# Performance work log

Hardware: AMD Instinct MI355X
Metric: run time of the kernel (lower is better)

The kernel has to match this reference:

```python
import jax, jax.numpy as jnp
import numpy as np

N_HEADS = 12  # from init_kwargs


def setup_inputs() -> dict:
    key = jax.random.key(0)
    ks = jax.random.split(key, 9)
    d_model = 768
    c, s = 50, 4          # n_classes, n_synonyms
    b, t = 4, 1024        # batch, document length
    scale = 0.02
    return {
        "Q": jax.random.normal(ks[0], (c, s, d_model), jnp.float32),
        "H": jax.random.normal(ks[1], (b, t, d_model), jnp.float32),
        "ql": jax.random.normal(ks[2], (c, d_model), jnp.float32),
        "WQ_w": jax.random.normal(ks[3], (d_model, d_model), jnp.float32) * scale,
        "WQ_b": jax.random.normal(ks[4], (d_model,), jnp.float32) * scale,
        "WK_w": jax.random.normal(ks[5], (d_model, d_model), jnp.float32) * scale,
        "WK_b": jax.random.normal(ks[6], (d_model,), jnp.float32) * scale,
        "WV_w": jax.random.normal(ks[7], (d_model, d_model), jnp.float32) * scale,
        "WV_b": jax.random.normal(ks[8], (d_model,), jnp.float32) * scale,
    }


def reference(Q, H, ql, WQ_w, WQ_b, WK_w, WK_b, WV_w, WV_b):
    c, s, d_model = Q.shape
    b, t, _ = H.shape
    z, h = N_HEADS, d_model // N_HEADS  # heads, d_k

    # projections + split heads
    q_s = (Q @ WQ_w + WQ_b).reshape(c, s, z, h).transpose(0, 2, 1, 3)   # [c,z,s,h]
    k_s = jnp.tanh((H @ WK_w + WK_b).reshape(b, t, z, h).transpose(0, 2, 1, 3))  # [b,z,t,h]
    Kh = jnp.tanh(H.reshape(b, t, z, h).transpose(0, 2, 1, 3))          # [b,z,t,h]

    # custom 5D attention
    scores = jnp.einsum('bzth,czsh->bczst', k_s, q_s)                   # [b,c,z,s,t]
    attn = jax.nn.softmax(scores, axis=-1)
    context = jnp.einsum('bzth,bczst->bczsh', Kh, attn)                 # [b,c,z,s,h]
    context = context.mean(axis=3)                                      # AvgPool3d over s -> [b,c,z,h]

    Wql = ql @ WV_w + WV_b                                               # [c,d_model]
    output = jnp.einsum('bch,ch->bc', context.reshape(b, c, z * h), Wql)
    return output
```

## Files before the change

### kernel.cpp

```cpp
#include <hip/hip_runtime.h>
#include <hip/hip_bf16.h>
#include <cmath>


typedef __attribute__((ext_vector_type(8))) short bf8_t;
typedef __attribute__((ext_vector_type(4))) float f32x4;

__device__ inline unsigned short f2bf(float x) {
    unsigned u = __float_as_uint(x);
    return (unsigned short)((u + 0x7fffu + ((u >> 16) & 1u)) >> 16);
}
__device__ inline float ftanh(float x) {
    float t = __expf(2.f * x);
    return 1.f - 2.f * __builtin_amdgcn_rcpf(t + 1.f);
}

__global__ __launch_bounds__(256) void prep_kernel(
    const float* __restrict__ H, const float* __restrict__ WK,
    const float* __restrict__ WQ, const float* __restrict__ WV,
    const float* __restrict__ Q, const float* __restrict__ ql,
    unsigned short* __restrict__ Hbf,
    unsigned short* __restrict__ WTk, unsigned short* __restrict__ WTq,
    unsigned short* __restrict__ WTv,
    unsigned short* __restrict__ Qbf, unsigned short* __restrict__ qlbf)
{
    __shared__ unsigned short tile[64][72];
    const int bid = blockIdx.x, tid = threadIdx.x;
    if (bid < 1536) {
        int i = (bid * 256 + tid) * 8;
        float4 v0 = *(const float4*)&H[i];
        float4 v1 = *(const float4*)&H[i + 4];
        unsigned short h8[8] = {f2bf(v0.x), f2bf(v0.y), f2bf(v0.z), f2bf(v0.w),
                                f2bf(v1.x), f2bf(v1.y), f2bf(v1.z), f2bf(v1.w)};
        *(bf8_t*)&Hbf[i] = *(const bf8_t*)h8;
    } else if (bid < 1968) {
        int j = bid - 1536;
        int wsel = j / 144, l = j % 144;
        const float* W = (wsel == 0) ? WK : (wsel == 1) ? WQ : WV;
        unsigned short* WT = (wsel == 0) ? WTk : (wsel == 1) ? WTq : WTv;
        const int bn = (l % 12) * 64, bk = (l / 12) * 64;
        const int k = tid >> 4, n4 = (tid & 15) << 2;
#pragma unroll
        for (int i = 0; i < 4; i++) {
            int kk = k + i * 16;
            float4 v = *(const float4*)&W[(size_t)(bk + kk) * 768 + bn + n4];
            tile[n4 + 0][kk] = f2bf(v.x);
            tile[n4 + 1][kk] = f2bf(v.y);
            tile[n4 + 2][kk] = f2bf(v.z);
            tile[n4 + 3][kk] = f2bf(v.w);
        }
        __syncthreads();
#pragma unroll
        for (int i = 0; i < 2; i++) {
            int idx = tid + i * 256;
            int n = idx >> 3, k8 = (idx & 7) << 3;
            *(bf8_t*)&WT[(size_t)(bn + n) * 768 + bk + k8] = *(const bf8_t*)&tile[n][k8];
        }
    } else if (bid < 2043) {
        int i = ((bid - 1968) * 256 + tid) * 8;
        float4 v0 = *(const float4*)&Q[i];
        float4 v1 = *(const float4*)&Q[i + 4];
        unsigned short h8[8] = {f2bf(v0.x), f2bf(v0.y), f2bf(v0.z), f2bf(v0.w),
                                f2bf(v1.x), f2bf(v1.y), f2bf(v1.z), f2bf(v1.w)};
        *(bf8_t*)&Qbf[i] = *(const bf8_t*)h8;
    } else {
        int i = ((bid - 2043) * 256 + tid) * 8;
        if (i < 38400) {
            float4 v0 = *(const float4*)&ql[i];
            float4 v1 = *(const float4*)&ql[i + 4];
            unsigned short h8[8] = {f2bf(v0.x), f2bf(v0.y), f2bf(v0.z), f2bf(v0.w),
                                    f2bf(v1.x), f2bf(v1.y), f2bf(v1.z), f2bf(v1.w)};
            *(bf8_t*)&qlbf[i] = *(const bf8_t*)h8;
        }
    }
}

__global__ __launch_bounds__(256) void gemm_all_kernel(
    const unsigned short* __restrict__ Hbf, const unsigned short* __restrict__ Qbf,
    const unsigned short* __restrict__ qlbf,
    const unsigned short* __restrict__ WTk, const unsigned short* __restrict__ WTq,
    const unsigned short* __restrict__ WTv,
    const float* __restrict__ bk, const float* __restrict__ bq,
    const float* __restrict__ bv,
    unsigned short* __restrict__ KSb, unsigned short* __restrict__ QSbf,
    unsigned short* __restrict__ WQLbf)
{
    __shared__ unsigned short Al[128][72];
    __shared__ unsigned short Bl[64][72];
    int bid = blockIdx.x;
    const int tid = threadIdx.x;
    if (bid < 384) bid = (bid & 7) * 48 + (bid >> 3);
    int job, bm, bn, Mr, z = 0;
    const unsigned short *A, *B;
    const float* bias;
    if (bid < 384) {
        job = 0; z = bid % 12; bm = (bid / 12) * 128; bn = z * 64;
        A = Hbf; B = WTk; bias = bk; Mr = 4096;
    } else if (bid < 408) {
        int l = bid - 384;
        job = 1; bm = (l / 12) * 128; bn = (l % 12) * 64;
        A = Qbf; B = WTq; bias = bq; Mr = 200;
    } else {
        job = 2; bm = 0; bn = (bid - 408) * 64;
        A = qlbf; B = WTv; bias = bv; Mr = 50;
    }
    const int lane = tid & 63, w = tid >> 6;
    const int wm = (w & 1) * 64, wn = (w >> 1) * 32;
    const int fr = lane & 15, fg = lane >> 4;

    f32x4 acc[4][2] = {};

    for (int k0 = 0; k0 < 768; k0 += 64) {
#pragma unroll
        for (int i = 0; i < 4; i++) {
            int f = tid + i * 256;
            int r = f >> 3, c8 = (f & 7) << 3;
            bf8_t v = {};
            if (bm + r < Mr)
                v = *(const bf8_t*)&A[(size_t)(bm + r) * 768 + k0 + c8];
            *(bf8_t*)&Al[r][c8] = v;
        }
#pragma unroll
        for (int i = 0; i < 2; i++) {
            int f = tid + i * 256;
            int r = f >> 3, c8 = (f & 7) << 3;
            *(bf8_t*)&Bl[r][c8] = *(const bf8_t*)&B[(size_t)(bn + r) * 768 + k0 + c8];
        }
        __syncthreads();
#pragma unroll
        for (int kk = 0; kk < 2; kk++) {
            bf8_t a[4], bb[2];
#pragma unroll
            for (int mt = 0; mt < 4; mt++)
                a[mt] = *(const bf8_t*)&Al[wm + mt * 16 + fr][kk * 32 + fg * 8];
#pragma unroll
            for (int nt = 0; nt < 2; nt++)
                bb[nt] = *(const bf8_t*)&Bl[wn + nt * 16 + fr][kk * 32 + fg * 8];
#pragma unroll
            for (int mt = 0; mt < 4; mt++)
#pragma unroll
                for (int nt = 0; nt < 2; nt++)
                    acc[mt][nt] = __builtin_amdgcn_mfma_f32_16x16x32_bf16(
                        a[mt], bb[nt], acc[mt][nt], 0, 0, 0);
        }
        __syncthreads();
    }
#pragma unroll
    for (int nt = 0; nt < 2; nt++) {
        int ng = bn + wn + nt * 16 + fr;
        float bvv = bias[ng];
        if (job == 0) {
            int hh = ng & 63;
#pragma unroll
            for (int mt = 0; mt < 4; mt++) {
#pragma unroll
                for (int r = 0; r < 4; r++) {
                    int rg = bm + wm + mt * 16 + fg * 4 + r;
                    int bb2 = rg >> 10, t = rg & 1023;
                    KSb[(((size_t)bb2 * 12 + z) * 1024 + t) * 64 + hh] =
                        f2bf(ftanh(acc[mt][nt][r] + bvv));
                }
            }
        } else {
            unsigned short* outp = (job == 1) ? QSbf : WQLbf;
            int Mw = (job == 1) ? 208 : 64;
#pragma unroll
            for (int mt = 0; mt < 4; mt++) {
#pragma unroll
                for (int r = 0; r < 4; r++) {
                    int rg = bm + wm + mt * 16 + fg * 4 + r;
                    if (rg < Mw)
                        outp[(size_t)rg * 768 + ng] = f2bf(acc[mt][nt][r] + bvv);
                }
            }
        }
    }
}

__global__ __launch_bounds__(256) void attn7_kernel(
    const unsigned short* __restrict__ KSb, const unsigned short* __restrict__ QSbf,
    const float* __restrict__ H, const unsigned short* __restrict__ WQLbf,
    float* __restrict__ pd, float* __restrict__ pn)
{
    __shared__ unsigned short KTl[128][72];
    __shared__ unsigned short Wl[64][72];
    __shared__ float kwl[128][50];
    const int blk = blockIdx.x;
    const int ts = blk & 7;
    const int z  = (blk >> 3) % 12;
    const int b  = blk / 96;
    const int tid = threadIdx.x;
    const int lane = tid & 63, w = tid >> 6;
    const int fr = lane & 15, fg = lane >> 4;

    const float* hb = H + ((size_t)(b * 1024 + ts * 128)) * 768 + z * 64;
#pragma unroll
    for (int i = 0; i < 4; i++) {
        int f = tid + i * 256;
        int r = f >> 3, c8 = (f & 7) << 3;
        float4 v0 = *(const float4*)&hb[(size_t)r * 768 + c8];
        float4 v1 = *(const float4*)&hb[(size_t)r * 768 + c8 + 4];
        unsigned short t8[8] = {f2bf(ftanh(v0.x)), f2bf(ftanh(v0.y)),
                                f2bf(ftanh(v0.z)), f2bf(ftanh(v0.w)),
                                f2bf(ftanh(v1.x)), f2bf(ftanh(v1.y)),
                                f2bf(ftanh(v1.z)), f2bf(ftanh(v1.w))};
        *(bf8_t*)&KTl[r][c8] = *(const bf8_t*)t8;
    }
#pragma unroll
    for (int i = 0; i < 2; i++) {
        int f = tid + i * 256;
        int r = f >> 3, c8 = (f & 7) << 3;
        *(bf8_t*)&Wl[r][c8] = *(const bf8_t*)&WQLbf[(size_t)r * 768 + z * 64 + c8];
    }
    __syncthreads();

    {
        const int wm = w * 32;
        f32x4 acc[2][4] = {};
#pragma unroll
        for (int kk = 0; kk < 2; kk++) {
            bf8_t a[2], bb[4];
#pragma unroll
            for (int mt = 0; mt < 2; mt++)
                a[mt] = *(const bf8_t*)&KTl[wm + mt * 16 + fr][kk * 32 + fg * 8];
#pragma unroll
            for (int nt = 0; nt < 4; nt++)
                bb[nt] = *(const bf8_t*)&Wl[nt * 16 + fr][kk * 32 + fg * 8];
#pragma unroll
            for (int mt = 0; mt < 2; mt++)
#pragma unroll
                for (int nt = 0; nt < 4; nt++)
                    acc[mt][nt] = __builtin_amdgcn_mfma_f32_16x16x32_bf16(
                        a[mt], bb[nt], acc[mt][nt], 0, 0, 0);
        }
#pragma unroll
        for (int nt = 0; nt < 4; nt++) {
            int c = nt * 16 + fr;
            if (c < 50) {
#pragma unroll
                for (int mt = 0; mt < 2; mt++)
#pragma unroll
                    for (int r = 0; r < 4; r++)
                        kwl[wm + mt * 16 + fg * 4 + r][c] = acc[mt][nt][r];
            }
        }
    }
    __syncthreads();

    const unsigned short* ksb = KSb + ((size_t)((b * 12 + z) * 1024) + ts * 128) * 64;
#pragma unroll
    for (int i = 0; i < 4; i++) {
        int f = tid + i * 256;
        int r = f >> 3, c8 = (f & 7) << 3;
        *(bf8_t*)&KTl[r][c8] = *(const bf8_t*)&ksb[(size_t)r * 64 + c8];
    }
    __syncthreads();

    bf8_t af[16];
#pragma unroll
    for (int mt = 0; mt < 8; mt++)
#pragma unroll
        for (int kk = 0; kk < 2; kk++)
            af[mt * 2 + kk] = *(const bf8_t*)&KTl[mt * 16 + fr][kk * 32 + fg * 8];

    for (int nt = w; nt < 13; nt += 4) {
        const int cs = nt * 16 + fr;
        const bool live = (cs < 200);
        const int kc = live ? (cs >> 2) : 0;
        bf8_t b0 = *(const bf8_t*)&QSbf[(size_t)(nt * 16 + fr) * 768 + z * 64 + fg * 8];
        bf8_t b1 = *(const bf8_t*)&QSbf[(size_t)(nt * 16 + fr) * 768 + z * 64 + 32 + fg * 8];

        float den = 0.f, num = 0.f;
#pragma unroll
        for (int mt = 0; mt < 8; mt++) {
            f32x4 acc = {};
            acc = __builtin_amdgcn_mfma_f32_16x16x32_bf16(af[mt * 2 + 0], b0, acc, 0, 0, 0);
            acc = __builtin_amdgcn_mfma_f32_16x16x32_bf16(af[mt * 2 + 1], b1, acc, 0, 0, 0);
#pragma unroll
            for (int j = 0; j < 4; j++) {
                float p = __expf(acc[j]);
                den += p;
                num += p * kwl[mt * 16 + fg * 4 + j][kc];
            }
        }
        den += __shfl_xor(den, 16); num += __shfl_xor(num, 16);
        den += __shfl_xor(den, 32); num += __shfl_xor(num, 32);
        if (fg == 0 && live) {
            size_t R = ((size_t)b * 200 + cs) * 12 + z;
            pd[R * 8 + ts] = den;
            pn[R * 8 + ts] = num;
        }
    }
}

__global__ __launch_bounds__(64) void reduce_kernel(
    const float* __restrict__ pd, const float* __restrict__ pn,
    float* __restrict__ out)
{
    const int bc = blockIdx.x;
    const int b = bc / 50, c = bc % 50;
    const int j = threadIdx.x;
    float ratio = 0.f;
    if (j < 48) {
        int zz = j >> 2, s = j & 3;
        size_t R = ((size_t)b * 200 + (c * 4 + s)) * 12 + zz;
        float D = 0.f, N = 0.f;
#pragma unroll
        for (int t = 0; t < 8; t++) {
            D += pd[R * 8 + t];
            N += pn[R * 8 + t];
        }
        ratio = N / D;
    }
#pragma unroll
    for (int off = 32; off; off >>= 1) ratio += __shfl_xor(ratio, off);
    if (j == 0) out[bc] = 0.25f * ratio;
}

extern "C" void kernel_launch(void* const* d_in, const int* in_sizes, int n_in,
                              void* d_out, int out_size, void* d_ws, size_t ws_size,
                              hipStream_t stream) {
    const float* Q    = (const float*)d_in[0];
    const float* H    = (const float*)d_in[1];
    const float* ql   = (const float*)d_in[2];
    const float* WQ_w = (const float*)d_in[3];
    const float* WQ_b = (const float*)d_in[4];
    const float* WK_w = (const float*)d_in[5];
    const float* WK_b = (const float*)d_in[6];
    const float* WV_w = (const float*)d_in[7];
    const float* WV_b = (const float*)d_in[8];
    float* out = (float*)d_out;

    float* ws = (float*)d_ws;
    unsigned short* KSb   = (unsigned short*)ws;
    unsigned short* Hbf   = (unsigned short*)(ws + 1572864);
    unsigned short* WTk   = (unsigned short*)(ws + 3145728);
    unsigned short* WTq   = (unsigned short*)(ws + 3440640);
    unsigned short* WTv   = (unsigned short*)(ws + 3735552);
    unsigned short* Qbf   = (unsigned short*)(ws + 4030464);
    unsigned short* qlbf  = (unsigned short*)(ws + 4107264);
    unsigned short* QSbf  = (unsigned short*)(ws + 4126464);
    unsigned short* WQLbf = (unsigned short*)(ws + 4206336);
    float* pd             = ws + 4230912;
    float* pn             = ws + 4307712;
    (void)in_sizes; (void)n_in; (void)out_size; (void)ws_size;

    prep_kernel<<<2062, 256, 0, stream>>>(H, WK_w, WQ_w, WV_w, Q, ql,
                                          Hbf, WTk, WTq, WTv, Qbf, qlbf);
    gemm_all_kernel<<<420, 256, 0, stream>>>(Hbf, Qbf, qlbf, WTk, WTq, WTv,
                                             WK_b, WQ_b, WV_b, KSb, QSbf, WQLbf);
    attn7_kernel<<<384, 256, 0, stream>>>(KSb, QSbf, H, WQLbf, pd, pn);
    reduce_kernel<<<200, 64, 0, stream>>>(pd, pn, out);
}
```

Measured before the change: 123.2 us.

## Fuse K projection into attention kernel and convert fp32 inputs to bf16 on load

The H@WK projection with tanh now runs inside the attention kernel, so the K tile stays in shared memory and is never written to or reread from global memory. The separate bf16 conversion passes for H, Q and ql are removed: these inputs are read as fp32 and rounded while being staged. The tanh(H) head slice is captured during the k-loop iteration that matches z and reused. This cuts global traffic and one launch, but the attention kernel now reads fp32 H and does the full GEMM, which adds latency per block and uses more LDS.

New measurement: 157.5 us. 1.28x slower.

```diff
diff --git a/kernel.cpp b/kernel.cpp
--- a/kernel.cpp
+++ b/kernel.cpp
@@ -10,115 +10,84 @@
     unsigned u = __float_as_uint(x);
     return (unsigned short)((u + 0x7fffu + ((u >> 16) & 1u)) >> 16);
 }
+__device__ inline float bf2f(unsigned short u) {
+    return __uint_as_float(((unsigned)u) << 16);
+}
 __device__ inline float ftanh(float x) {
     float t = __expf(2.f * x);
     return 1.f - 2.f * __builtin_amdgcn_rcpf(t + 1.f);
 }
 
 __global__ __launch_bounds__(256) void prep_kernel(
-    const float* __restrict__ H, const float* __restrict__ WK,
-    const float* __restrict__ WQ, const float* __restrict__ WV,
-    const float* __restrict__ Q, const float* __restrict__ ql,
-    unsigned short* __restrict__ Hbf,
+    const float* __restrict__ WK, const float* __restrict__ WQ,
+    const float* __restrict__ WV,
     unsigned short* __restrict__ WTk, unsigned short* __restrict__ WTq,
-    unsigned short* __restrict__ WTv,
-    unsigned short* __restrict__ Qbf, unsigned short* __restrict__ qlbf)
+    unsigned short* __restrict__ WTv)
 {
     __shared__ unsigned short tile[64][72];
     const int bid = blockIdx.x, tid = threadIdx.x;
-    if (bid < 1536) {
-        int i = (bid * 256 + tid) * 8;
-        float4 v0 = *(const float4*)&H[i];
-        float4 v1 = *(const float4*)&H[i + 4];
-        unsigned short h8[8] = {f2bf(v0.x), f2bf(v0.y), f2bf(v0.z), f2bf(v0.w),
-                                f2bf(v1.x), f2bf(v1.y), f2bf(v1.z), f2bf(v1.w)};
-        *(bf8_t*)&Hbf[i] = *(const bf8_t*)h8;
-    } else if (bid < 1968) {
-        int j = bid - 1536;
-        int wsel = j / 144, l = j % 144;
-        const float* W = (wsel == 0) ? WK : (wsel == 1) ? WQ : WV;
-        unsigned short* WT = (wsel == 0) ? WTk : (wsel == 1) ? WTq : WTv;
-        const int bn = (l % 12) * 64, bk = (l / 12) * 64;
-        const int k = tid >> 4, n4 = (tid & 15) << 2;
-#pragma unroll
-        for (int i = 0; i < 4; i++) {
-            int kk = k + i * 16;
-            float4 v = *(const float4*)&W[(size_t)(bk + kk) * 768 + bn + n4];
-            tile[n4 + 0][kk] = f2bf(v.x);
-            tile[n4 + 1][kk] = f2bf(v.y);
-            tile[n4 + 2][kk] = f2bf(v.z);
-            tile[n4 + 3][kk] = f2bf(v.w);
-        }
-        __syncthreads();
-#pragma unroll
-        for (int i = 0; i < 2; i++) {
-            int idx = tid + i * 256;
-            int n = idx >> 3, k8 = (idx & 7) << 3;
-            *(bf8_t*)&WT[(size_t)(bn + n) * 768 + bk + k8] = *(const bf8_t*)&tile[n][k8];
-        }
-    } else if (bid < 2043) {
-        int i = ((bid - 1968) * 256 + tid) * 8;
-        float4 v0 = *(const float4*)&Q[i];
-        float4 v1 = *(const float4*)&Q[i + 4];
-        unsigned short h8[8] = {f2bf(v0.x), f2bf(v0.y), f2bf(v0.z), f2bf(v0.w),
-                                f2bf(v1.x), f2bf(v1.y), f2bf(v1.z), f2bf(v1.w)};
-        *(bf8_t*)&Qbf[i] = *(const bf8_t*)h8;
-    } else {
-        int i = ((bid - 2043) * 256 + tid) * 8;
-        if (i < 38400) {
-            float4 v0 = *(const float4*)&ql[i];
-            float4 v1 = *(const float4*)&ql[i + 4];
-            unsigned short h8[8] = {f2bf(v0.x), f2bf(v0.y), f2bf(v0.z), f2bf(v0.w),
-                                    f2bf(v1.x), f2bf(v1.y), f2bf(v1.z), f2bf(v1.w)};
-            *(bf8_t*)&qlbf[i] = *(const bf8_t*)h8;
-        }
-    }
-}
-
-__global__ __launch_bounds__(256) void gemm_all_kernel(
-    const unsigned short* __restrict__ Hbf, const unsigned short* __restrict__ Qbf,
-    const unsigned short* __restrict__ qlbf,
-    const unsigned short* __restrict__ WTk, const unsigned short* __restrict__ WTq,
-    const unsigned short* __restrict__ WTv,
-    const float* __restrict__ bk, const float* __restrict__ bq,
-    const float* __restrict__ bv,
-    unsigned short* __restrict__ KSb, unsigned short* __restrict__ QSbf,
-    unsigned short* __restrict__ WQLbf)
+    const int wsel = bid / 144, l = bid % 144;
+    const float* W = (wsel == 0) ? WK : (wsel == 1) ? WQ : WV;
+    unsigned short* WT = (wsel == 0) ? WTk : (wsel == 1) ? WTq : WTv;
+    const int bn = (l % 12) * 64, bk = (l / 12) * 64;
+    const int k = tid >> 4, n4 = (tid & 15) << 2;
+#pragma unroll
+    for (int i = 0; i < 4; i++) {
+        int kk = k + i * 16;
+        float4 v = *(const float4*)&W[(size_t)(bk + kk) * 768 + bn + n4];
+        tile[n4 + 0][kk] = f2bf(v.x);
+        tile[n4 + 1][kk] = f2bf(v.y);
+        tile[n4 + 2][kk] = f2bf(v.z);
+        tile[n4 + 3][kk] = f2bf(v.w);
+    }
+    __syncthreads();
+#pragma unroll
+    for (int i = 0; i < 2; i++) {
+        int idx = tid + i * 256;
+        int n = idx >> 3, k8 = (idx & 7) << 3;
+        *(bf8_t*)&WT[(size_t)(bn + n) * 768 + bk + k8] = *(const bf8_t*)&tile[n][k8];
+    }
+}
+
+__global__ __launch_bounds__(256) void gemm_qs_kernel(
+    const float* __restrict__ Q, const float* __restrict__ ql,
+    const unsigned short* __restrict__ WTq, const unsigned short* __restrict__ WTv,
+    const float* __restrict__ bq, const float* __restrict__ bv,
+    unsigned short* __restrict__ QSbf, unsigned short* __restrict__ WQLbf)
 {
     __shared__ unsigned short Al[128][72];
     __shared__ unsigned short Bl[64][72];
-    int bid = blockIdx.x;
-    const int tid = threadIdx.x;
-    if (bid < 384) bid = (bid & 7) * 48 + (bid >> 3);
-    int job, bm, bn, Mr, z = 0;
-    const unsigned short *A, *B;
+    const int bid = blockIdx.x, tid = threadIdx.x;
+    int bm, bn, Mr, Mw;
+    const float* A;
+    const unsigned short* B;
     const float* bias;
-    if (bid < 384) {
-        job = 0; z = bid % 12; bm = (bid / 12) * 128; bn = z * 64;
-        A = Hbf; B = WTk; bias = bk; Mr = 4096;
-    } else if (bid < 408) {
-        int l = bid - 384;
-        job = 1; bm = (l / 12) * 128; bn = (l % 12) * 64;
-        A = Qbf; B = WTq; bias = bq; Mr = 200;
+    unsigned short* outp;
+    if (bid < 24) {
+        bm = (bid / 12) * 128; bn = (bid % 12) * 64;
+        A = Q; B = WTq; bias = bq; Mr = 200; Mw = 208; outp = QSbf;
     } else {
-        job = 2; bm = 0; bn = (bid - 408) * 64;
-        A = qlbf; B = WTv; bias = bv; Mr = 50;
+        bm = 0; bn = (bid - 24) * 64;
+        A = ql; B = WTv; bias = bv; Mr = 50; Mw = 64; outp = WQLbf;
     }
     const int lane = tid & 63, w = tid >> 6;
     const int wm = (w & 1) * 64, wn = (w >> 1) * 32;
     const int fr = lane & 15, fg = lane >> 4;
 
     f32x4 acc[4][2] = {};
-
     for (int k0 = 0; k0 < 768; k0 += 64) {
 #pragma unroll
         for (int i = 0; i < 4; i++) {
             int f = tid + i * 256;
             int r = f >> 3, c8 = (f & 7) << 3;
-            bf8_t v = {};
-            if (bm + r < Mr)
-                v = *(const bf8_t*)&A[(size_t)(bm + r) * 768 + k0 + c8];
-            *(bf8_t*)&Al[r][c8] = v;
+            unsigned short t8[8] = {0, 0, 0, 0, 0, 0, 0, 0};
+            if (bm + r < Mr) {
+                float4 v0 = *(const float4*)&A[(size_t)(bm + r) * 768 + k0 + c8];
+                float4 v1 = *(const float4*)&A[(size_t)(bm + r) * 768 + k0 + c8 + 4];
+                t8[0] = f2bf(v0.x); t8[1] = f2bf(v0.y); t8[2] = f2bf(v0.z); t8[3] = f2bf(v0.w);
+                t8[4] = f2bf(v1.x); t8[5] = f2bf(v1.y); t8[6] = f2bf(v1.z); t8[7] = f2bf(v1.w);
+            }
+            *(bf8_t*)&Al[r][c8] = *(const bf8_t*)t8;
         }
 #pragma unroll
         for (int i = 0; i < 2; i++) {
@@ -149,90 +118,129 @@
     for (int nt = 0; nt < 2; nt++) {
         int ng = bn + wn + nt * 16 + fr;
         float bvv = bias[ng];
-        if (job == 0) {
-            int hh = ng & 63;
-#pragma unroll
-            for (int mt = 0; mt < 4; mt++) {
-#pragma unroll
-                for (int r = 0; r < 4; r++) {
-                    int rg = bm + wm + mt * 16 + fg * 4 + r;
-                    int bb2 = rg >> 10, t = rg & 1023;
-                    KSb[(((size_t)bb2 * 12 + z) * 1024 + t) * 64 + hh] =
-                        f2bf(ftanh(acc[mt][nt][r] + bvv));
-                }
+#pragma unroll
+        for (int mt = 0; mt < 4; mt++)
+#pragma unroll
+            for (int r = 0; r < 4; r++) {
+                int rg = bm + wm + mt * 16 + fg * 4 + r;
+                if (rg < Mw)
+                    outp[(size_t)rg * 768 + ng] = f2bf(acc[mt][nt][r] + bvv);
             }
-        } else {
-            unsigned short* outp = (job == 1) ? QSbf : WQLbf;
-            int Mw = (job == 1) ? 208 : 64;
-#pragma unroll
-            for (int mt = 0; mt < 4; mt++) {
-#pragma unroll
-                for (int r = 0; r < 4; r++) {
-                    int rg = bm + wm + mt * 16 + fg * 4 + r;
-                    if (rg < Mw)
-                        outp[(size_t)rg * 768 + ng] = f2bf(acc[mt][nt][r] + bvv);
-                }
-            }
-        }
-    }
-}
-
-__global__ __launch_bounds__(256) void attn7_kernel(
-    const unsigned short* __restrict__ KSb, const unsigned short* __restrict__ QSbf,
-    const float* __restrict__ H, const unsigned short* __restrict__ WQLbf,
+    }
+}
+
+__global__ __launch_bounds__(256) void attn_mega_kernel(
+    const float* __restrict__ H, const unsigned short* __restrict__ WTk,
+    const float* __restrict__ bk,
+    const unsigned short* __restrict__ QSbf, const unsigned short* __restrict__ WQLbf,
     float* __restrict__ pd, float* __restrict__ pn)
 {
-    __shared__ unsigned short KTl[128][72];
-    __shared__ unsigned short Wl[64][72];
-    __shared__ float kwl[128][50];
-    const int blk = blockIdx.x;
-    const int ts = blk & 7;
-    const int z  = (blk >> 3) % 12;
-    const int b  = blk / 96;
+    __shared__ __align__(16) unsigned short pool[23040];
+    unsigned short (*Al)[72]  = (unsigned short (*)[72])(pool);
+    unsigned short (*THl)[72] = (unsigned short (*)[72])(pool + 9216);
+    unsigned short (*Bl)[72]  = (unsigned short (*)[72])(pool + 18432);
+    float (*kwl)[50]          = (float (*)[50])(pool + 9216);
+
+    int bid = blockIdx.x;
+    bid = (bid & 7) * 48 + (bid >> 3);
+    const int z = bid % 12;
+    const int g = bid / 12;
+    const int b = g >> 3, ts = g & 7;
     const int tid = threadIdx.x;
     const int lane = tid & 63, w = tid >> 6;
+    const int wm = (w & 1) * 64, wn = (w >> 1) * 32;
     const int fr = lane & 15, fg = lane >> 4;
-
-    const float* hb = H + ((size_t)(b * 1024 + ts * 128)) * 768 + z * 64;
+    const size_t hrow = (size_t)(b * 1024 + ts * 128);
+
+    f32x4 acc[4][2] = {};
+    for (int k0 = 0; k0 < 768; k0 += 64) {
+        const bool cap = (k0 == z * 64);
+#pragma unroll
+        for (int i = 0; i < 4; i++) {
+            int f = tid + i * 256;
+            int r = f >> 3, c8 = (f & 7) << 3;
+            float4 v0 = *(const float4*)&H[(hrow + r) * 768 + k0 + c8];
+            float4 v1 = *(const float4*)&H[(hrow + r) * 768 + k0 + c8 + 4];
+            unsigned short t8[8] = {f2bf(v0.x), f2bf(v0.y), f2bf(v0.z), f2bf(v0.w),
+                                    f2bf(v1.x), f2bf(v1.y), f2bf(v1.z), f2bf(v1.w)};
+            *(bf8_t*)&Al[r][c8] = *(const bf8_t*)t8;
+            if (cap) *(bf8_t*)&THl[r][c8] = *(const bf8_t*)t8;
+        }
+#pragma unroll
+        for (int i = 0; i < 2; i++) {
+            int f = tid + i * 256;
+            int r = f >> 3, c8 = (f & 7) << 3;
+            *(bf8_t*)&Bl[r][c8] = *(const bf8_t*)&WTk[(size_t)(z * 64 + r) * 768 + k0 + c8];
+        }
+        __syncthreads();
+#pragma unroll
+        for (int kk = 0; kk < 2; kk++) {
+            bf8_t a[4], bb[2];
+#pragma unroll
+            for (int mt = 0; mt < 4; mt++)
+                a[mt] = *(const bf8_t*)&Al[wm + mt * 16 + fr][kk * 32 + fg * 8];
+#pragma unroll
+            for (int nt = 0; nt < 2; nt++)
+                bb[nt] = *(const bf8_t*)&Bl[wn + nt * 16 + fr][kk * 32 + fg * 8];
+#pragma unroll
+            for (int mt = 0; mt < 4; mt++)
+#pragma unroll
+                for (int nt = 0; nt < 2; nt++)
+                    acc[mt][nt] = __builtin_amdgcn_mfma_f32_16x16x32_bf16(
+                        a[mt], bb[nt], acc[mt][nt], 0, 0, 0);
+        }
+        __syncthreads();
+    }
+
+#pragma unroll
+    for (int nt = 0; nt < 2; nt++) {
+        int hh = wn + nt * 16 + fr;
+        float bvv = bk[z * 64 + hh];
+#pragma unroll
+        for (int mt = 0; mt < 4; mt++)
+#pragma unroll
+            for (int r = 0; r < 4; r++)
+                Al[wm + mt * 16 + fg * 4 + r][hh] = f2bf(ftanh(acc[mt][nt][r] + bvv));
+    }
 #pragma unroll
     for (int i = 0; i < 4; i++) {
         int f = tid + i * 256;
         int r = f >> 3, c8 = (f & 7) << 3;
-        float4 v0 = *(const float4*)&hb[(size_t)r * 768 + c8];
-        float4 v1 = *(const float4*)&hb[(size_t)r * 768 + c8 + 4];
-        unsigned short t8[8] = {f2bf(ftanh(v0.x)), f2bf(ftanh(v0.y)),
-                                f2bf(ftanh(v0.z)), f2bf(ftanh(v0.w)),
-                                f2bf(ftanh(v1.x)), f2bf(ftanh(v1.y)),
-                                f2bf(ftanh(v1.z)), f2bf(ftanh(v1.w))};
-        *(bf8_t*)&KTl[r][c8] = *(const bf8_t*)t8;
+        bf8_t v = *(const bf8_t*)&THl[r][c8];
+        unsigned short t8[8];
+#pragma unroll
+        for (int j = 0; j < 8; j++)
+            t8[j] = f2bf(ftanh(bf2f((unsigned short)v[j])));
+        *(bf8_t*)&THl[r][c8] = *(const bf8_t*)t8;
     }
 #pragma unroll
     for (int i = 0; i < 2; i++) {
         int f = tid + i * 256;
         int r = f >> 3, c8 = (f & 7) << 3;
-        *(bf8_t*)&Wl[r][c8] = *(const bf8_t*)&WQLbf[(size_t)r * 768 + z * 64 + c8];
+        *(bf8_t*)&Bl[r][c8] = *(const bf8_t*)&WQLbf[(size_t)r * 768 + z * 64 + c8];
     }
     __syncthreads();
 
     {
-        const int wm = w * 32;
-        f32x4 acc[2][4] = {};
+        const int wm2 = w * 32;
+        f32x4 a1[2][4] = {};
 #pragma unroll
         for (int kk = 0; kk < 2; kk++) {
             bf8_t a[2], bb[4];
 #pragma unroll
             for (int mt = 0; mt < 2; mt++)
-                a[mt] = *(const bf8_t*)&KTl[wm + mt * 16 + fr][kk * 32 + fg * 8];
+                a[mt] = *(const bf8_t*)&THl[wm2 + mt * 16 + fr][kk * 32 + fg * 8];
 #pragma unroll
             for (int nt = 0; nt < 4; nt++)
-                bb[nt] = *(const bf8_t*)&Wl[nt * 16 + fr][kk * 32 + fg * 8];
+                bb[nt] = *(const bf8_t*)&Bl[nt * 16 + fr][kk * 32 + fg * 8];
 #pragma unroll
             for (int mt = 0; mt < 2; mt++)
 #pragma unroll
                 for (int nt = 0; nt < 4; nt++)
-                    acc[mt][nt] = __builtin_amdgcn_mfma_f32_16x16x32_bf16(
-                        a[mt], bb[nt], acc[mt][nt], 0, 0, 0);
-        }
+                    a1[mt][nt] = __builtin_amdgcn_mfma_f32_16x16x32_bf16(
+                        a[mt], bb[nt], a1[mt][nt], 0, 0, 0);
+        }
+        __syncthreads();
 #pragma unroll
         for (int nt = 0; nt < 4; nt++) {
             int c = nt * 16 + fr;
@@ -241,27 +249,18 @@
                 for (int mt = 0; mt < 2; mt++)
 #pragma unroll
                     for (int r = 0; r < 4; r++)
-                        kwl[wm + mt * 16 + fg * 4 + r][c] = acc[mt][nt][r];
+                        kwl[wm2 + mt * 16 + fg * 4 + r][c] = a1[mt][nt][r];
             }
         }
     }
     __syncthreads();
 
-    const unsigned short* ksb = KSb + ((size_t)((b * 12 + z) * 1024) + ts * 128) * 64;
-#pragma unroll
-    for (int i = 0; i < 4; i++) {
-        int f = tid + i * 256;
-        int r = f >> 3, c8 = (f & 7) << 3;
-        *(bf8_t*)&KTl[r][c8] = *(const bf8_t*)&ksb[(size_t)r * 64 + c8];
-    }
-    __syncthreads();
-
     bf8_t af[16];
 #pragma unroll
     for (int mt = 0; mt < 8; mt++)
 #pragma unroll
         for (int kk = 0; kk < 2; kk++)
-            af[mt * 2 + kk] = *(const bf8_t*)&KTl[mt * 16 + fr][kk * 32 + fg * 8];
+            af[mt * 2 + kk] = *(const bf8_t*)&Al[mt * 16 + fr][kk * 32 + fg * 8];
 
     for (int nt = w; nt < 13; nt += 4) {
         const int cs = nt * 16 + fr;
@@ -273,12 +272,12 @@
         float den = 0.f, num = 0.f;
 #pragma unroll
         for (int mt = 0; mt < 8; mt++) {
-            f32x4 acc = {};
-            acc = __builtin_amdgcn_mfma_f32_16x16x32_bf16(af[mt * 2 + 0], b0, acc, 0, 0, 0);
-            acc = __builtin_amdgcn_mfma_f32_16x16x32_bf16(af[mt * 2 + 1], b1, acc, 0, 0, 0);
+            f32x4 sc = {};
+            sc = __builtin_amdgcn_mfma_f32_16x16x32_bf16(af[mt * 2 + 0], b0, sc, 0, 0, 0);
+            sc = __builtin_amdgcn_mfma_f32_16x16x32_bf16(af[mt * 2 + 1], b1, sc, 0, 0, 0);
 #pragma unroll
             for (int j = 0; j < 4; j++) {
-                float p = __expf(acc[j]);
+                float p = __expf(sc[j]);
                 den += p;
                 num += p * kwl[mt * 16 + fg * 4 + j][kc];
             }
@@ -332,23 +331,17 @@
     float* out = (float*)d_out;
 
     float* ws = (float*)d_ws;
-    unsigned short* KSb   = (unsigned short*)ws;
-    unsigned short* Hbf   = (unsigned short*)(ws + 1572864);
-    unsigned short* WTk   = (unsigned short*)(ws + 3145728);
-    unsigned short* WTq   = (unsigned short*)(ws + 3440640);
-    unsigned short* WTv   = (unsigned short*)(ws + 3735552);
-    unsigned short* Qbf   = (unsigned short*)(ws + 4030464);
-    unsigned short* qlbf  = (unsigned short*)(ws + 4107264);
-    unsigned short* QSbf  = (unsigned short*)(ws + 4126464);
-    unsigned short* WQLbf = (unsigned short*)(ws + 4206336);
-    float* pd             = ws + 4230912;
-    float* pn             = ws + 4307712;
+    unsigned short* WTk   = (unsigned short*)ws;
+    unsigned short* WTq   = (unsigned short*)(ws + 294912);
+    unsigned short* WTv   = (unsigned short*)(ws + 589824);
+    unsigned short* QSbf  = (unsigned short*)(ws + 884736);
+    unsigned short* WQLbf = (unsigned short*)(ws + 964608);
+    float* pd             = ws + 989184;
+    float* pn             = ws + 1065984;
     (void)in_sizes; (void)n_in; (void)out_size; (void)ws_size;
 
-    prep_kernel<<<2062, 256, 0, stream>>>(H, WK_w, WQ_w, WV_w, Q, ql,
-                                          Hbf, WTk, WTq, WTv, Qbf, qlbf);
-    gemm_all_kernel<<<420, 256, 0, stream>>>(Hbf, Qbf, qlbf, WTk, WTq, WTv,
-                                             WK_b, WQ_b, WV_b, KSb, QSbf, WQLbf);
-    attn7_kernel<<<384, 256, 0, stream>>>(KSb, QSbf, H, WQLbf, pd, pn);
+    prep_kernel<<<432, 256, 0, stream>>>(WK_w, WQ_w, WV_w, WTk, WTq, WTv);
+    gemm_qs_kernel<<<36, 256, 0, stream>>>(Q, ql, WTq, WTv, WQ_b, WV_b, QSbf, WQLbf);
+    attn_mega_kernel<<<384, 256, 0, stream>>>(H, WTk, WK_b, QSbf, WQLbf, pd, pn);
     reduce_kernel<<<200, 64, 0, stream>>>(pd, pn, out);
 }
```

## Halve GEMM and attention tiles, fuse Q/ql conversion, read bf16 H in attention

Applied to the files above, without the earlier changes.

The GEMM and attention kernels now use 64-row tiles instead of 128, which doubles the grid to fill more CUs. The partial-sum split in the reduce step grows from 8 to 16 chunks. The Q and ql fp32-to-bf16 conversion moves out of the prep kernel and into the GEMM A-load, which removes two intermediate buffers. Attention now reads the bf16 copy of H instead of fp32 H, halving that traffic. The cost is a slight precision change in tanh(H), since its input is now rounded to bf16 first, plus more redundant B-tile loads and more partial sums.

Result: no change. 121.3 us (-1.6%).

```diff
diff --git a/kernel.cpp b/kernel.cpp
--- a/kernel.cpp
+++ b/kernel.cpp
@@ -10,6 +10,9 @@
     unsigned u = __float_as_uint(x);
     return (unsigned short)((u + 0x7fffu + ((u >> 16) & 1u)) >> 16);
 }
+__device__ inline float bf2f(unsigned short u) {
+    return __uint_as_float(((unsigned)u) << 16);
+}
 __device__ inline float ftanh(float x) {
     float t = __expf(2.f * x);
     return 1.f - 2.f * __builtin_amdgcn_rcpf(t + 1.f);
@@ -18,11 +21,9 @@
 __global__ __launch_bounds__(256) void prep_kernel(
     const float* __restrict__ H, const float* __restrict__ WK,
     const float* __restrict__ WQ, const float* __restrict__ WV,
-    const float* __restrict__ Q, const float* __restrict__ ql,
     unsigned short* __restrict__ Hbf,
     unsigned short* __restrict__ WTk, unsigned short* __restrict__ WTq,
-    unsigned short* __restrict__ WTv,
-    unsigned short* __restrict__ Qbf, unsigned short* __restrict__ qlbf)
+    unsigned short* __restrict__ WTv)
 {
     __shared__ unsigned short tile[64][72];
     const int bid = blockIdx.x, tid = threadIdx.x;
@@ -33,7 +34,7 @@
         unsigned short h8[8] = {f2bf(v0.x), f2bf(v0.y), f2bf(v0.z), f2bf(v0.w),
                                 f2bf(v1.x), f2bf(v1.y), f2bf(v1.z), f2bf(v1.w)};
         *(bf8_t*)&Hbf[i] = *(const bf8_t*)h8;
-    } else if (bid < 1968) {
+    } else {
         int j = bid - 1536;
         int wsel = j / 144, l = j % 144;
         const float* W = (wsel == 0) ? WK : (wsel == 1) ? WQ : WV;
@@ -56,28 +57,12 @@
             int n = idx >> 3, k8 = (idx & 7) << 3;
             *(bf8_t*)&WT[(size_t)(bn + n) * 768 + bk + k8] = *(const bf8_t*)&tile[n][k8];
         }
-    } else if (bid < 2043) {
-        int i = ((bid - 1968) * 256 + tid) * 8;
-        float4 v0 = *(const float4*)&Q[i];
-        float4 v1 = *(const float4*)&Q[i + 4];
-        unsigned short h8[8] = {f2bf(v0.x), f2bf(v0.y), f2bf(v0.z), f2bf(v0.w),
-                                f2bf(v1.x), f2bf(v1.y), f2bf(v1.z), f2bf(v1.w)};
-        *(bf8_t*)&Qbf[i] = *(const bf8_t*)h8;
-    } else {
-        int i = ((bid - 2043) * 256 + tid) * 8;
-        if (i < 38400) {
-            float4 v0 = *(const float4*)&ql[i];
-            float4 v1 = *(const float4*)&ql[i + 4];
-            unsigned short h8[8] = {f2bf(v0.x), f2bf(v0.y), f2bf(v0.z), f2bf(v0.w),
-                                    f2bf(v1.x), f2bf(v1.y), f2bf(v1.z), f2bf(v1.w)};
-            *(bf8_t*)&qlbf[i] = *(const bf8_t*)h8;
-        }
     }
 }
 
 __global__ __launch_bounds__(256) void gemm_all_kernel(
-    const unsigned short* __restrict__ Hbf, const unsigned short* __restrict__ Qbf,
-    const unsigned short* __restrict__ qlbf,
+    const unsigned short* __restrict__ Hbf,
+    const float* __restrict__ Q, const float* __restrict__ ql,
     const unsigned short* __restrict__ WTk, const unsigned short* __restrict__ WTq,
     const unsigned short* __restrict__ WTv,
     const float* __restrict__ bk, const float* __restrict__ bq,
@@ -85,40 +70,51 @@
     unsigned short* __restrict__ KSb, unsigned short* __restrict__ QSbf,
     unsigned short* __restrict__ WQLbf)
 {
-    __shared__ unsigned short Al[128][72];
+    __shared__ unsigned short Al[64][72];
     __shared__ unsigned short Bl[64][72];
     int bid = blockIdx.x;
     const int tid = threadIdx.x;
-    if (bid < 384) bid = (bid & 7) * 48 + (bid >> 3);
-    int job, bm, bn, Mr, z = 0;
-    const unsigned short *A, *B;
+    if (bid < 768) bid = (bid & 7) * 96 + (bid >> 3);
+    int job, bm, bn, Mr = 0, Mw = 0, z = 0;
+    const float* Af = nullptr;
+    const unsigned short* B;
     const float* bias;
-    if (bid < 384) {
-        job = 0; z = bid % 12; bm = (bid / 12) * 128; bn = z * 64;
-        A = Hbf; B = WTk; bias = bk; Mr = 4096;
-    } else if (bid < 408) {
-        int l = bid - 384;
-        job = 1; bm = (l / 12) * 128; bn = (l % 12) * 64;
-        A = Qbf; B = WTq; bias = bq; Mr = 200;
+    if (bid < 768) {
+        job = 0; z = bid % 12; bm = (bid / 12) * 64; bn = z * 64;
+        B = WTk; bias = bk;
+    } else if (bid < 816) {
+        int l = bid - 768;
+        job = 1; bm = (l / 12) * 64; bn = (l % 12) * 64;
+        Af = Q; B = WTq; bias = bq; Mr = 200; Mw = 208;
     } else {
-        job = 2; bm = 0; bn = (bid - 408) * 64;
-        A = qlbf; B = WTv; bias = bv; Mr = 50;
+        job = 2; bm = 0; bn = (bid - 816) * 64;
+        Af = ql; B = WTv; bias = bv; Mr = 50; Mw = 64;
     }
     const int lane = tid & 63, w = tid >> 6;
-    const int wm = (w & 1) * 64, wn = (w >> 1) * 32;
+    const int wm = (w & 1) * 32, wn = (w >> 1) * 32;
     const int fr = lane & 15, fg = lane >> 4;
 
-    f32x4 acc[4][2] = {};
-
+    f32x4 acc[2][2] = {};
     for (int k0 = 0; k0 < 768; k0 += 64) {
 #pragma unroll
-        for (int i = 0; i < 4; i++) {
+        for (int i = 0; i < 2; i++) {
             int f = tid + i * 256;
             int r = f >> 3, c8 = (f & 7) << 3;
-            bf8_t v = {};
-            if (bm + r < Mr)
-                v = *(const bf8_t*)&A[(size_t)(bm + r) * 768 + k0 + c8];
-            *(bf8_t*)&Al[r][c8] = v;
+            if (job == 0) {
+                *(bf8_t*)&Al[r][c8] =
+                    *(const bf8_t*)&Hbf[(size_t)(bm + r) * 768 + k0 + c8];
+            } else {
+                unsigned short t8[8] = {0, 0, 0, 0, 0, 0, 0, 0};
+                if (bm + r < Mr) {
+                    float4 v0 = *(const float4*)&Af[(size_t)(bm + r) * 768 + k0 + c8];
+                    float4 v1 = *(const float4*)&Af[(size_t)(bm + r) * 768 + k0 + c8 + 4];
+                    t8[0] = f2bf(v0.x); t8[1] = f2bf(v0.y);
+                    t8[2] = f2bf(v0.z); t8[3] = f2bf(v0.w);
+                    t8[4] = f2bf(v1.x); t8[5] = f2bf(v1.y);
+                    t8[6] = f2bf(v1.z); t8[7] = f2bf(v1.w);
+                }
+                *(bf8_t*)&Al[r][c8] = *(const bf8_t*)t8;
+            }
         }
 #pragma unroll
         for (int i = 0; i < 2; i++) {
@@ -129,15 +125,15 @@
         __syncthreads();
 #pragma unroll
         for (int kk = 0; kk < 2; kk++) {
-            bf8_t a[4], bb[2];
-#pragma unroll
-            for (int mt = 0; mt < 4; mt++)
+            bf8_t a[2], bb[2];
+#pragma unroll
+            for (int mt = 0; mt < 2; mt++)
                 a[mt] = *(const bf8_t*)&Al[wm + mt * 16 + fr][kk * 32 + fg * 8];
 #pragma unroll
             for (int nt = 0; nt < 2; nt++)
                 bb[nt] = *(const bf8_t*)&Bl[wn + nt * 16 + fr][kk * 32 + fg * 8];
 #pragma unroll
-            for (int mt = 0; mt < 4; mt++)
+            for (int mt = 0; mt < 2; mt++)
 #pragma unroll
                 for (int nt = 0; nt < 2; nt++)
                     acc[mt][nt] = __builtin_amdgcn_mfma_f32_16x16x32_bf16(
@@ -152,7 +148,7 @@
         if (job == 0) {
             int hh = ng & 63;
 #pragma unroll
-            for (int mt = 0; mt < 4; mt++) {
+            for (int mt = 0; mt < 2; mt++) {
 #pragma unroll
                 for (int r = 0; r < 4; r++) {
                     int rg = bm + wm + mt * 16 + fg * 4 + r;
@@ -163,9 +159,8 @@
             }
         } else {
             unsigned short* outp = (job == 1) ? QSbf : WQLbf;
-            int Mw = (job == 1) ? 208 : 64;
-#pragma unroll
-            for (int mt = 0; mt < 4; mt++) {
+#pragma unroll
+            for (int mt = 0; mt < 2; mt++) {
 #pragma unroll
                 for (int r = 0; r < 4; r++) {
                     int rg = bm + wm + mt * 16 + fg * 4 + r;
@@ -179,31 +174,30 @@
 
 __global__ __launch_bounds__(256) void attn7_kernel(
     const unsigned short* __restrict__ KSb, const unsigned short* __restrict__ QSbf,
-    const float* __restrict__ H, const unsigned short* __restrict__ WQLbf,
+    const unsigned short* __restrict__ Hbf, const unsigned short* __restrict__ WQLbf,
     float* __restrict__ pd, float* __restrict__ pn)
 {
-    __shared__ unsigned short KTl[128][72];
+    __shared__ unsigned short KTl[64][72];
     __shared__ unsigned short Wl[64][72];
-    __shared__ float kwl[128][50];
+    __shared__ float kwl[64][50];
     const int blk = blockIdx.x;
-    const int ts = blk & 7;
-    const int z  = (blk >> 3) % 12;
-    const int b  = blk / 96;
+    const int ts = blk & 15;
+    const int z  = (blk >> 4) % 12;
+    const int b  = blk / 192;
     const int tid = threadIdx.x;
     const int lane = tid & 63, w = tid >> 6;
     const int fr = lane & 15, fg = lane >> 4;
 
-    const float* hb = H + ((size_t)(b * 1024 + ts * 128)) * 768 + z * 64;
-#pragma unroll
-    for (int i = 0; i < 4; i++) {
+    const unsigned short* hb = Hbf + (size_t)(b * 1024 + ts * 64) * 768 + z * 64;
+#pragma unroll
+    for (int i = 0; i < 2; i++) {
         int f = tid + i * 256;
         int r = f >> 3, c8 = (f & 7) << 3;
-        float4 v0 = *(const float4*)&hb[(size_t)r * 768 + c8];
-        float4 v1 = *(const float4*)&hb[(size_t)r * 768 + c8 + 4];
-        unsigned short t8[8] = {f2bf(ftanh(v0.x)), f2bf(ftanh(v0.y)),
-                                f2bf(ftanh(v0.z)), f2bf(ftanh(v0.w)),
-                                f2bf(ftanh(v1.x)), f2bf(ftanh(v1.y)),
-                                f2bf(ftanh(v1.z)), f2bf(ftanh(v1.w))};
+        bf8_t v = *(const bf8_t*)&hb[(size_t)r * 768 + c8];
+        unsigned short t8[8];
+#pragma unroll
+        for (int j = 0; j < 8; j++)
+            t8[j] = f2bf(ftanh(bf2f((unsigned short)v[j])));
         *(bf8_t*)&KTl[r][c8] = *(const bf8_t*)t8;
     }
 #pragma unroll
@@ -215,50 +209,41 @@
     __syncthreads();
 
     {
-        const int wm = w * 32;
-        f32x4 acc[2][4] = {};
+        const int wm2 = w * 16;
+        f32x4 a1[4] = {};
 #pragma unroll
         for (int kk = 0; kk < 2; kk++) {
-            bf8_t a[2], bb[4];
-#pragma unroll
-            for (int mt = 0; mt < 2; mt++)
-                a[mt] = *(const bf8_t*)&KTl[wm + mt * 16 + fr][kk * 32 + fg * 8];
-#pragma unroll
-            for (int nt = 0; nt < 4; nt++)
-                bb[nt] = *(const bf8_t*)&Wl[nt * 16 + fr][kk * 32 + fg * 8];
-#pragma unroll
-            for (int mt = 0; mt < 2; mt++)
-#pragma unroll
-                for (int nt = 0; nt < 4; nt++)
-                    acc[mt][nt] = __builtin_amdgcn_mfma_f32_16x16x32_bf16(
-                        a[mt], bb[nt], acc[mt][nt], 0, 0, 0);
+            bf8_t a = *(const bf8_t*)&KTl[wm2 + fr][kk * 32 + fg * 8];
+#pragma unroll
+            for (int nt = 0; nt < 4; nt++) {
+                bf8_t bb = *(const bf8_t*)&Wl[nt * 16 + fr][kk * 32 + fg * 8];
+                a1[nt] = __builtin_amdgcn_mfma_f32_16x16x32_bf16(a, bb, a1[nt], 0, 0, 0);
+            }
         }
 #pragma unroll
         for (int nt = 0; nt < 4; nt++) {
             int c = nt * 16 + fr;
             if (c < 50) {
 #pragma unroll
-                for (int mt = 0; mt < 2; mt++)
-#pragma unroll
-                    for (int r = 0; r < 4; r++)
-                        kwl[wm + mt * 16 + fg * 4 + r][c] = acc[mt][nt][r];
+                for (int r = 0; r < 4; r++)
+                    kwl[wm2 + fg * 4 + r][c] = a1[nt][r];
             }
         }
     }
     __syncthreads();
 
-    const unsigned short* ksb = KSb + ((size_t)((b * 12 + z) * 1024) + ts * 128) * 64;
-#pragma unroll
-    for (int i = 0; i < 4; i++) {
+    const unsigned short* ksb = KSb + ((size_t)((b * 12 + z) * 1024) + ts * 64) * 64;
+#pragma unroll
+    for (int i = 0; i < 2; i++) {
         int f = tid + i * 256;
         int r = f >> 3, c8 = (f & 7) << 3;
         *(bf8_t*)&KTl[r][c8] = *(const bf8_t*)&ksb[(size_t)r * 64 + c8];
     }
     __syncthreads();
 
-    bf8_t af[16];
-#pragma unroll
-    for (int mt = 0; mt < 8; mt++)
+    bf8_t af[8];
+#pragma unroll
+    for (int mt = 0; mt < 4; mt++)
 #pragma unroll
         for (int kk = 0; kk < 2; kk++)
             af[mt * 2 + kk] = *(const bf8_t*)&KTl[mt * 16 + fr][kk * 32 + fg * 8];
@@ -272,13 +257,13 @@
 
         float den = 0.f, num = 0.f;
 #pragma unroll
-        for (int mt = 0; mt < 8; mt++) {
-            f32x4 acc = {};
-            acc = __builtin_amdgcn_mfma_f32_16x16x32_bf16(af[mt * 2 + 0], b0, acc, 0, 0, 0);
-            acc = __builtin_amdgcn_mfma_f32_16x16x32_bf16(af[mt * 2 + 1], b1, acc, 0, 0, 0);
+        for (int mt = 0; mt < 4; mt++) {
+            f32x4 sc = {};
+            sc = __builtin_amdgcn_mfma_f32_16x16x32_bf16(af[mt * 2 + 0], b0, sc, 0, 0, 0);
+            sc = __builtin_amdgcn_mfma_f32_16x16x32_bf16(af[mt * 2 + 1], b1, sc, 0, 0, 0);
 #pragma unroll
             for (int j = 0; j < 4; j++) {
-                float p = __expf(acc[j]);
+                float p = __expf(sc[j]);
                 den += p;
                 num += p * kwl[mt * 16 + fg * 4 + j][kc];
             }
@@ -287,8 +272,8 @@
         den += __shfl_xor(den, 32); num += __shfl_xor(num, 32);
         if (fg == 0 && live) {
             size_t R = ((size_t)b * 200 + cs) * 12 + z;
-            pd[R * 8 + ts] = den;
-            pn[R * 8 + ts] = num;
+            pd[R * 16 + ts] = den;
+            pn[R * 16 + ts] = num;
         }
     }
 }
@@ -306,9 +291,9 @@
         size_t R = ((size_t)b * 200 + (c * 4 + s)) * 12 + zz;
         float D = 0.f, N = 0.f;
 #pragma unroll
-        for (int t = 0; t < 8; t++) {
-            D += pd[R * 8 + t];
-            N += pn[R * 8 + t];
+        for (int t = 0; t < 16; t++) {
+            D += pd[R * 16 + t];
+            N += pn[R * 16 + t];
         }
         ratio = N / D;
     }
@@ -332,23 +317,20 @@
     float* out = (float*)d_out;
 
     float* ws = (float*)d_ws;
-    unsigned short* KSb   = (unsigned short*)ws;
-    unsigned short* Hbf   = (unsigned short*)(ws + 1572864);
-    unsigned short* WTk   = (unsigned short*)(ws + 3145728);
-    unsigned short* WTq   = (unsigned short*)(ws + 3440640);
-    unsigned short* WTv   = (unsigned short*)(ws + 3735552);
-    unsigned short* Qbf   = (unsigned short*)(ws + 4030464);
-    unsigned short* qlbf  = (unsigned short*)(ws + 4107264);
-    unsigned short* QSbf  = (unsigned short*)(ws + 4126464);
-    unsigned short* WQLbf = (unsigned short*)(ws + 4206336);
-    float* pd             = ws + 4230912;
-    float* pn             = ws + 4307712;
+    unsigned short* WTk   = (unsigned short*)ws;
+    unsigned short* WTq   = (unsigned short*)(ws + 294912);
+    unsigned short* WTv   = (unsigned short*)(ws + 589824);
+    unsigned short* Hbf   = (unsigned short*)(ws + 884736);
+    unsigned short* KSb   = (unsigned short*)(ws + 2457600);
+    unsigned short* QSbf  = (unsigned short*)(ws + 4030464);
+    unsigned short* WQLbf = (unsigned short*)(ws + 4110336);
+    float* pd             = ws + 4134912;
+    float* pn             = ws + 4288512;
     (void)in_sizes; (void)n_in; (void)out_size; (void)ws_size;
 
-    prep_kernel<<<2062, 256, 0, stream>>>(H, WK_w, WQ_w, WV_w, Q, ql,
-                                          Hbf, WTk, WTq, WTv, Qbf, qlbf);
-    gemm_all_kernel<<<420, 256, 0, stream>>>(Hbf, Qbf, qlbf, WTk, WTq, WTv,
+    prep_kernel<<<1968, 256, 0, stream>>>(H, WK_w, WQ_w, WV_w, Hbf, WTk, WTq, WTv);
+    gemm_all_kernel<<<828, 256, 0, stream>>>(Hbf, Q, ql, WTk, WTq, WTv,
                                              WK_b, WQ_b, WV_b, KSb, QSbf, WQLbf);
-    attn7_kernel<<<384, 256, 0, stream>>>(KSb, QSbf, H, WQLbf, pd, pn);
+    attn7_kernel<<<768, 256, 0, stream>>>(KSb, QSbf, Hbf, WQLbf, pd, pn);
     reduce_kernel<<<200, 64, 0, stream>>>(pd, pn, out);
 }
```
